# Performance work log

Hardware: AMD Instinct MI355X
Metric: run time of the kernel (lower is better)

The kernel has to match this reference:

```python
import jax, jax.numpy as jnp
import numpy as np

B, S, H, E, K = 4, 2048, 1024, 8, 2

def setup_inputs() -> dict:
    key = jax.random.key(0)
    k0, k1, k2, k3 = jax.random.split(key, 4)
    x = jax.random.normal(k0, (B, S, H), dtype=jnp.float32)
    # xavier-uniform-like scales
    router_w = jax.random.normal(k1, (E, H), dtype=jnp.float32) * np.float32(1.0 / np.sqrt(H))
    xav1 = np.float32(np.sqrt(2.0 / (2 * H + H)))
    w1 = jax.random.normal(k2, (E, 2 * H, H), dtype=jnp.float32) * xav1
    w2 = jax.random.normal(k3, (E, H, 2 * H), dtype=jnp.float32) * xav1
    return {"x": x, "router_w": router_w, "w1": w1, "w2": w2}

def reference(x, router_w, w1, w2):
    bsz, seq, hidden = x.shape
    n_experts = w1.shape[0]
    tokens = x.reshape(-1, hidden)                      # [T, H]
    T = tokens.shape[0]
    logits = tokens @ router_w.T                        # [T, E]
    topv, topi = jax.lax.top_k(logits, K)               # [T, K]
    w = jax.nn.softmax(topv, axis=-1).astype(tokens.dtype)
    # Dense gate matrix: gate[t, e] = routing weight of expert e for token t
    # (zero for non-selected experts). Equivalent to the torch pad/dispatch/
    # scatter-add combine: padded slots have weight 0 and contribute nothing.
    gate = jnp.zeros((T, n_experts), tokens.dtype).at[jnp.arange(T)[:, None], topi].add(w)
    out = jnp.zeros_like(tokens)
    for e in range(n_experts):  # small fixed expert count
        h = jax.nn.gelu(tokens @ w1[e].T, approximate=False)  # [T, 2H] (torch F.gelu = erf)
        y = h @ w2[e].T                                       # [T, H]
        out = out + gate[:, e:e + 1] * y
    return out.reshape(bsz, seq, hidden)
```

## Files before the change

### kernel.cpp

```cpp
#include <hip/hip_runtime.h>
#include <stdint.h>
#include <math.h>

#define T_TOK 8192
#define H_DIM 1024
#define H2    2048
#define NE    8

typedef unsigned short u16;
typedef __attribute__((ext_vector_type(8))) short bf16x8;
typedef __attribute__((ext_vector_type(4))) float f32x4;

__device__ __forceinline__ u16 f32_to_bf16(float f) {
  union { float f; unsigned u; } c; c.f = f;
  unsigned u = c.u + 0x7fffu + ((c.u >> 16) & 1u);
  return (u16)(u >> 16);
}
__device__ __forceinline__ float bf2f(u16 v) {
  union { unsigned u; float f; } c; c.u = (unsigned)v << 16; return c.f;
}

__device__ __forceinline__ float fast_gelu(float v) {
  float u = v * v;
  float z2 = v * fmaf(u, 0.1029437f, 2.3022078f);
  float e = __builtin_amdgcn_exp2f(z2);
  float r = __builtin_amdgcn_rcpf(1.0f + e);
  return v - v * r;
}

__device__ __forceinline__ void g2l16(const void* g, void* l) {
  __builtin_amdgcn_global_load_lds(
      (const __attribute__((address_space(1))) unsigned*)g,
      (__attribute__((address_space(3))) unsigned*)l, 16, 0, 0);
}

__device__ __forceinline__ int prefix_base(const int* counts, int e) {
  int b = 0;
#pragma unroll
  for (int j = 0; j < NE; j++) b += (j < e) ? counts[j] : 0;
  return b;
}

__global__ __launch_bounds__(256) void prep_kernel(
    const float* __restrict__ x, const float* __restrict__ rw,
    const float* __restrict__ w1, const float* __restrict__ w2,
    u16* __restrict__ xb, u16* __restrict__ w1b, u16* __restrict__ w2b,
    int* __restrict__ tope, float2* __restrict__ gate2,
    int* __restrict__ counts) {
  int blk = blockIdx.x;
  if (blk < T_TOK / 4) {
    int wave = threadIdx.x >> 6;
    int lane = threadIdx.x & 63;
    int t = blk * 4 + wave;
    const float4* x4 = (const float4*)(x + (size_t)t * H_DIM);
    const float4* rw4 = (const float4*)rw;
    u16* xbrow = xb + (size_t)t * H_DIM;

    double acc[NE];
#pragma unroll
    for (int e = 0; e < NE; e++) acc[e] = 0.0;
#pragma unroll
    for (int i = 0; i < 4; i++) {
      int c = lane + 64 * i;
      float4 xv = x4[c];
      ushort4 bv = make_ushort4(f32_to_bf16(xv.x), f32_to_bf16(xv.y),
                                f32_to_bf16(xv.z), f32_to_bf16(xv.w));
      *(ushort4*)(xbrow + c * 4) = bv;
#pragma unroll
      for (int e = 0; e < NE; e++) {
        float4 wv = rw4[e * 256 + c];
        acc[e] += (double)xv.x * wv.x + (double)xv.y * wv.y +
                  (double)xv.z * wv.z + (double)xv.w * wv.w;
      }
    }
#pragma unroll
    for (int off = 32; off >= 1; off >>= 1)
#pragma unroll
      for (int e = 0; e < NE; e++) acc[e] += __shfl_xor(acc[e], off, 64);

    if (lane == 0) {
      int e0 = 0; double v0 = acc[0];
#pragma unroll
      for (int e = 1; e < NE; e++) if (acc[e] > v0) { v0 = acc[e]; e0 = e; }
      int e1 = -1; double v1 = -1e300;
#pragma unroll
      for (int e = 0; e < NE; e++) if (e != e0 && acc[e] > v1) { v1 = acc[e]; e1 = e; }
      double ex = exp(v1 - v0);
      tope[t] = e0 | (e1 << 8);
      gate2[t] = make_float2((float)(1.0 / (1.0 + ex)), (float)(ex / (1.0 + ex)));
    }
  } else {
    int cb = blk - T_TOK / 4;
    if (cb == 0 && threadIdx.x < NE) counts[threadIdx.x] = 0;
    const float* src; u16* dst;
    if (cb < 3072) { src = w1; dst = w1b; }
    else           { src = w2; dst = w2b; cb -= 3072; }
    const int n4 = NE * H2 * H_DIM / 4;
    const int stride = 3072 * 256;
    const float4* s4 = (const float4*)src;
    for (int i = cb * 256 + threadIdx.x; i < n4; i += stride) {
      float4 v = s4[i];
      *(ushort4*)(dst + (size_t)i * 4) = make_ushort4(
          f32_to_bf16(v.x), f32_to_bf16(v.y), f32_to_bf16(v.z), f32_to_bf16(v.w));
    }
  }
}

__global__ __launch_bounds__(256) void build_kernel(
    const int* __restrict__ tope, int* __restrict__ counts,
    int* __restrict__ tok_list, int2* __restrict__ pos2) {
  __shared__ int cts[4][NE];
  __shared__ int gbase[NE];
  int tid = threadIdx.x, lane = tid & 63, w = tid >> 6;
  int t = blockIdx.x * 256 + tid;
  int pk = tope[t];
  int e0 = pk & 0xff, e1 = (pk >> 8) & 0xff;
  unsigned long long lt = ((unsigned long long)1 << lane) - 1;

  int r0 = 0, r1 = 0;
#pragma unroll
  for (int e = 0; e < NE; e++) {
    unsigned long long b0 = __ballot(e0 == e);
    unsigned long long b1 = __ballot(e1 == e);
    int n0 = __popcll(b0), n1 = __popcll(b1);
    if (e0 == e) r0 = __popcll(b0 & lt);
    if (e1 == e) r1 = n0 + __popcll(b1 & lt);
    if (lane == 0) cts[w][e] = n0 + n1;
  }
  __syncthreads();
  if (tid < NE) {
    int bt = cts[0][tid] + cts[1][tid] + cts[2][tid] + cts[3][tid];
    gbase[tid] = atomicAdd(&counts[tid], bt);
  }
  __syncthreads();
  int off0 = gbase[e0] + r0;
  int off1 = gbase[e1] + r1;
#pragma unroll
  for (int wp = 0; wp < 4; wp++) {
    if (wp < w) { off0 += cts[wp][e0]; off1 += cts[wp][e1]; }
  }
  tok_list[e0 * T_TOK + off0] = t;
  tok_list[e1 * T_TOK + off1] = t;
  pos2[t] = make_int2(off0, off1);
}

template <int NK, int NT, int OUTN, bool GATHER, bool GELU>
__global__ __launch_bounds__(512, 2) void moe_gemm(
    const u16* __restrict__ A, const u16* __restrict__ W,
    u16* __restrict__ O, const int* __restrict__ tok_list,
    const int* __restrict__ counts) {
  const int MTMAX = T_TOK / 256;
  int e = blockIdx.x / (MTMAX * NT);
  int rem = blockIdx.x % (MTMAX * NT);
  int mt = rem / NT, nt = rem % NT;
  int cnt = counts[e];
  int m0 = mt * 256;
  if (m0 >= cnt) return;
  int base = prefix_base(counts, e);
  const int K = NK * 32;

  __shared__ u16 lA[4][8192];
  __shared__ u16 lB[4][8192];

  int tid = threadIdx.x;
  int lane = tid & 63, wave = tid >> 6;
  int wr = wave >> 2, wc = wave & 3;
  int quad = lane >> 4, l16 = lane & 15;

  int cg = (tid & 3) ^ ((tid >> 3) & 3);
  const u16* We = W + (size_t)e * OUTN * K;
  const u16* asrc[2]; const u16* bsrc[2];
#pragma unroll
  for (int r = 0; r < 2; ++r) {
    int row = (tid >> 2) + 128 * r;
    int ar = m0 + row; if (ar > cnt - 1) ar = cnt - 1;
    if (GATHER) asrc[r] = A + (size_t)tok_list[e * T_TOK + ar] * K + cg * 8;
    else        asrc[r] = A + (size_t)(base + ar) * K + cg * 8;
    bsrc[r] = We + (size_t)(nt * 256 + row) * K + cg * 8;
  }

  auto stage = [&](int kt) {
    int b = kt & 3;
#pragma unroll
    for (int r = 0; r < 2; ++r) {
      g2l16(asrc[r] + kt * 32, &lA[b][r * 4096 + tid * 8]);
      g2l16(bsrc[r] + kt * 32, &lB[b][r * 4096 + tid * 8]);
    }
  };

  f32x4 acc[8][4];
#pragma unroll
  for (int i = 0; i < 8; i++)
#pragma unroll
    for (int j = 0; j < 4; j++)
#pragma unroll
      for (int r = 0; r < 4; r++) acc[i][j][r] = 0.f;

  stage(0); stage(1); stage(2);
  asm volatile("s_waitcnt vmcnt(8)" ::: "memory");
  __builtin_amdgcn_s_barrier();
  __builtin_amdgcn_sched_barrier(0);

  int aoff = (wr * 128 + l16) * 32 + (quad ^ ((l16 >> 1) & 3)) * 8;
  int boff = (wc * 64 + l16) * 32 + (quad ^ ((l16 >> 1) & 3)) * 8;

#pragma unroll 1
  for (int k = 0; k < NK; ++k) {
    const u16* Ab = &lA[k & 3][0] + aoff;
    const u16* Bb = &lB[k & 3][0] + boff;
    bf16x8 af[8], bfr[4];
#pragma unroll
    for (int mi = 0; mi < 8; ++mi)
      af[mi] = *(const bf16x8*)(Ab + mi * 512);
#pragma unroll
    for (int ni = 0; ni < 4; ++ni)
      bfr[ni] = *(const bf16x8*)(Bb + ni * 512);

    if (k + 3 < NK) stage(k + 3);

    __builtin_amdgcn_s_setprio(1);
#pragma unroll
    for (int mi = 0; mi < 8; ++mi)
#pragma unroll
      for (int ni = 0; ni < 4; ++ni)
        acc[mi][ni] = __builtin_amdgcn_mfma_f32_16x16x32_bf16(
            af[mi], bfr[ni], acc[mi][ni], 0, 0, 0);
    __builtin_amdgcn_s_setprio(0);

    if (k + 3 < NK)      asm volatile("s_waitcnt vmcnt(8)" ::: "memory");
    else if (k + 2 < NK) asm volatile("s_waitcnt vmcnt(4)" ::: "memory");
    else if (k + 1 < NK) asm volatile("s_waitcnt vmcnt(0)" ::: "memory");
    if (k + 1 < NK) {
      __builtin_amdgcn_s_barrier();
      __builtin_amdgcn_sched_barrier(0);
    }
  }

#pragma unroll
  for (int mi = 0; mi < 8; ++mi) {
    int rb = wr * 128 + mi * 16 + quad * 4;
#pragma unroll
    for (int r = 0; r < 4; ++r) {
      int grow = m0 + rb + r;
      if (grow < cnt) {
        size_t o = (size_t)(base + grow) * OUTN + nt * 256 + wc * 64 + l16;
#pragma unroll
        for (int ni = 0; ni < 4; ++ni) {
          float v = acc[mi][ni][r];
          if (GELU) v = fast_gelu(v);
          O[o + ni * 16] = f32_to_bf16(v);
        }
      }
    }
  }
}

__global__ __launch_bounds__(256) void combine_kernel(
    const u16* __restrict__ y, const int* __restrict__ tope,
    const float2* __restrict__ gate2, const int2* __restrict__ pos2,
    const int* __restrict__ counts, float* __restrict__ out) {
  int t = blockIdx.x;
  int pk = tope[t];
  int e0 = pk & 0xff, e1 = (pk >> 8) & 0xff;
  float2 g = gate2[t];
  int2 p = pos2[t];
  int hb0 = prefix_base(counts, e0);
  int hb1 = prefix_base(counts, e1);
  size_t s0 = (size_t)(hb0 + p.x) * H_DIM + threadIdx.x * 4;
  size_t s1 = (size_t)(hb1 + p.y) * H_DIM + threadIdx.x * 4;
  ushort4 a = *(const ushort4*)(y + s0);
  ushort4 b = *(const ushort4*)(y + s1);
  float4 o;
  o.x = g.x * bf2f(a.x) + g.y * bf2f(b.x);
  o.y = g.x * bf2f(a.y) + g.y * bf2f(b.y);
  o.z = g.x * bf2f(a.z) + g.y * bf2f(b.z);
  o.w = g.x * bf2f(a.w) + g.y * bf2f(b.w);
  *(float4*)(out + (size_t)t * H_DIM + threadIdx.x * 4) = o;
}

extern "C" void kernel_launch(void* const* d_in, const int* in_sizes, int n_in,
                              void* d_out, int out_size, void* d_ws, size_t ws_size,
                              hipStream_t stream) {
  const float* x  = (const float*)d_in[0];
  const float* rw = (const float*)d_in[1];
  const float* w1 = (const float*)d_in[2];
  const float* w2 = (const float*)d_in[3];
  float* out = (float*)d_out;

  char* ws = (char*)d_ws;
  u16* xb       = (u16*)(ws);
  u16* w1b      = (u16*)(ws + 16777216);
  u16* y        = (u16*)(ws + 16777216);
  u16* w2b      = (u16*)(ws + 50331648);
  u16* h        = (u16*)(ws + 83886080);
  int* tok_list = (int*)(ws + 150994944);
  int* tope     = (int*)(ws + 151257088);
  float2* gate2 = (float2*)(ws + 151289856);
  int2* pos2    = (int2*)(ws + 151355392);
  int* counts   = (int*)(ws + 151420928);

  prep_kernel<<<T_TOK / 4 + 6144, 256, 0, stream>>>(x, rw, w1, w2, xb, w1b, w2b,
                                                    tope, gate2, counts);
  build_kernel<<<T_TOK / 256, 256, 0, stream>>>(tope, counts, tok_list, pos2);
  moe_gemm<32, 8, H2, true, true>
      <<<NE * 32 * 8, 512, 0, stream>>>(xb, w1b, h, tok_list, counts);
  moe_gemm<64, 4, H_DIM, false, false>
      <<<NE * 32 * 4, 512, 0, stream>>>(h, w2b, y, tok_list, counts);
  combine_kernel<<<T_TOK, 256, 0, stream>>>(y, tope, gate2, pos2, counts, out);
}
```

Measured before the change: 400.8 us.

## Restructure expert GEMM main loop into half-tile double-buffered ping-pong schedule

The expert GEMM now uses 64-wide K tiles and two LDS buffers, each split into halves, replacing the previous 4-stage ring of 32-wide K tiles. Each K tile is processed as four quarter MFMA blocks. Global-to-LDS loads for later halves are issued between these blocks, with barriers fencing each block, so memory traffic overlaps compute at a finer grain. LDS addressing uses a new XOR swizzle over 8 chunks per row. The change adds many more barriers per tile and relies on precise vmcnt accounting, which could cost more in synchronisation than the overlap gains.

```diff
diff --git a/kernel.cpp b/kernel.cpp
--- a/kernel.cpp
+++ b/kernel.cpp
@@ -144,7 +144,66 @@
   pos2[t] = make_int2(off0, off1);
 }
 
-template <int NK, int NT, int OUTN, bool GATHER, bool GELU>
+#define SB  __builtin_amdgcn_sched_barrier(0)
+#define BAR() do { SB; __builtin_amdgcn_s_barrier(); SB; } while (0)
+#define VMW(N) asm volatile("s_waitcnt vmcnt(" #N ")" ::: "memory")
+
+#define LDA(D,H,F,KK) (*(const bf16x8*)&lA[(((D)*2+(H))<<13) + adA[F][KK]])
+#define LDB(D,H,J,KK) (*(const bf16x8*)&lB[(((D)*2+(H))<<13) + adB[J][KK]])
+
+#define RDA(D,H) do { _Pragma("unroll") \
+  for (int f_ = 0; f_ < 4; ++f_) { af[f_][0] = LDA(D,H,f_,0); af[f_][1] = LDA(D,H,f_,1); } } while (0)
+#define RDB(D,H,BP) do { \
+  BP[0][0]=LDB(D,H,0,0); BP[0][1]=LDB(D,H,0,1); \
+  BP[1][0]=LDB(D,H,1,0); BP[1][1]=LDB(D,H,1,1); } while (0)
+
+#define STGA(D,H,KT) do { \
+  g2l16(aptr[H][0] + (KT)*64, &lA[(((D)*2+(H))<<13) + sd0]); \
+  g2l16(aptr[H][1] + (KT)*64, &lA[(((D)*2+(H))<<13) + sd1]); } while (0)
+#define STGB(D,H,KT) do { \
+  g2l16(bptr[H][0] + (KT)*64, &lB[(((D)*2+(H))<<13) + sd0]); \
+  g2l16(bptr[H][1] + (KT)*64, &lB[(((D)*2+(H))<<13) + sd1]); } while (0)
+
+#define MMQ(FB, BP, NB) do { \
+  __builtin_amdgcn_s_setprio(1); \
+  _Pragma("unroll") \
+  for (int f_ = 0; f_ < 4; ++f_) \
+    _Pragma("unroll") \
+    for (int j_ = 0; j_ < 2; ++j_) \
+      _Pragma("unroll") \
+      for (int k_ = 0; k_ < 2; ++k_) \
+        acc[(FB)+f_][(NB)+j_] = __builtin_amdgcn_mfma_f32_16x16x32_bf16( \
+            af[f_][k_], BP[j_][k_], acc[(FB)+f_][(NB)+j_], 0, 0, 0); \
+  __builtin_amdgcn_s_setprio(0); \
+} while (0)
+
+#define TILE_FULL(D, KT) do { \
+  RDA(D,0); RDB(D,0,b0); SB; STGA(((D)^1), 1, (KT)+1); \
+  BAR(); MMQ(0, b0, 0); BAR(); \
+  RDB(D,1,b1); SB; STGA(D, 0, (KT)+2); \
+  BAR(); MMQ(0, b1, 2); BAR(); \
+  RDA(D,1); SB; STGB(D, 0, (KT)+2); \
+  BAR(); MMQ(4, b0, 0); BAR(); \
+  SB; STGB(D, 1, (KT)+2); \
+  BAR(); MMQ(4, b1, 2); VMW(6); BAR(); \
+} while (0)
+
+#define TILE_TAIL1(D, KT) do { \
+  RDA(D,0); RDB(D,0,b0); SB; STGA(((D)^1), 1, (KT)+1); \
+  BAR(); MMQ(0, b0, 0); BAR(); \
+  RDB(D,1,b1); BAR(); MMQ(0, b1, 2); BAR(); \
+  RDA(D,1); BAR(); MMQ(4, b0, 0); BAR(); \
+  MMQ(4, b1, 2); VMW(0); BAR(); \
+} while (0)
+
+#define TILE_TAIL0(D) do { \
+  RDA(D,0); RDB(D,0,b0); BAR(); MMQ(0, b0, 0); BAR(); \
+  RDB(D,1,b1); BAR(); MMQ(0, b1, 2); BAR(); \
+  RDA(D,1); BAR(); MMQ(4, b0, 0); BAR(); \
+  MMQ(4, b1, 2); \
+} while (0)
+
+template <int NKT, int NT, int OUTN, bool GATHER, bool GELU>
 __global__ __launch_bounds__(512, 2) void moe_gemm(
     const u16* __restrict__ A, const u16* __restrict__ W,
     u16* __restrict__ O, const int* __restrict__ tok_list,
@@ -157,36 +216,53 @@
   int m0 = mt * 256;
   if (m0 >= cnt) return;
   int base = prefix_base(counts, e);
-  const int K = NK * 32;
-
-  __shared__ u16 lA[4][8192];
-  __shared__ u16 lB[4][8192];
+  const int K = NKT * 64;
+
+  __shared__ u16 lA[32768];
+  __shared__ u16 lB[32768];
 
   int tid = threadIdx.x;
-  int lane = tid & 63, wave = tid >> 6;
-  int wr = wave >> 2, wc = wave & 3;
-  int quad = lane >> 4, l16 = lane & 15;
-
-  int cg = (tid & 3) ^ ((tid >> 3) & 3);
+  int ln = tid & 63, w = tid >> 6;
+  int wr = w >> 2, wc = w & 3;
+  int quad = ln >> 4, l16 = ln & 15;
+
+  int sd0 = w * 1024 + ln * 8;
+  int sd1 = sd0 + 512;
   const u16* We = W + (size_t)e * OUTN * K;
-  const u16* asrc[2]; const u16* bsrc[2];
-#pragma unroll
-  for (int r = 0; r < 2; ++r) {
-    int row = (tid >> 2) + 128 * r;
-    int ar = m0 + row; if (ar > cnt - 1) ar = cnt - 1;
-    if (GATHER) asrc[r] = A + (size_t)tok_list[e * T_TOK + ar] * K + cg * 8;
-    else        asrc[r] = A + (size_t)(base + ar) * K + cg * 8;
-    bsrc[r] = We + (size_t)(nt * 256 + row) * K + cg * 8;
-  }
-
-  auto stage = [&](int kt) {
-    int b = kt & 3;
-#pragma unroll
-    for (int r = 0; r < 2; ++r) {
-      g2l16(asrc[r] + kt * 32, &lA[b][r * 4096 + tid * 8]);
-      g2l16(bsrc[r] + kt * 32, &lB[b][r * 4096 + tid * 8]);
-    }
-  };
+  const u16* aptr[2][2]; const u16* bptr[2][2];
+#pragma unroll
+  for (int c = 0; c < 2; ++c) {
+    int j16 = w * 128 + c * 64 + ln;
+    int lr = j16 >> 3;
+    int chunk = (j16 & 7) ^ (lr & 7);
+#pragma unroll
+    for (int h = 0; h < 2; ++h) {
+      int arow = ((lr >> 6) << 7) + h * 64 + (lr & 63);
+      int ar = m0 + arow; if (ar > cnt - 1) ar = cnt - 1;
+      const u16* ab;
+      if (GATHER) ab = A + (size_t)tok_list[e * T_TOK + ar] * K;
+      else        ab = A + (size_t)(base + ar) * K;
+      aptr[h][c] = ab + chunk * 8;
+      int brow = ((lr >> 5) << 6) + h * 32 + (lr & 31);
+      bptr[h][c] = We + (size_t)(nt * 256 + brow) * K + chunk * 8;
+    }
+  }
+
+  int adA[4][2], adB[2][2];
+#pragma unroll
+  for (int f = 0; f < 4; ++f) {
+    int lr = wr * 64 + f * 16 + l16;
+#pragma unroll
+    for (int kk = 0; kk < 2; ++kk)
+      adA[f][kk] = lr * 64 + ((((kk << 2) | quad) ^ (lr & 7)) << 3);
+  }
+#pragma unroll
+  for (int j = 0; j < 2; ++j) {
+    int lr = wc * 32 + j * 16 + l16;
+#pragma unroll
+    for (int kk = 0; kk < 2; ++kk)
+      adB[j][kk] = lr * 64 + ((((kk << 2) | quad) ^ (lr & 7)) << 3);
+  }
 
   f32x4 acc[8][4];
 #pragma unroll
@@ -196,45 +272,20 @@
 #pragma unroll
       for (int r = 0; r < 4; r++) acc[i][j][r] = 0.f;
 
-  stage(0); stage(1); stage(2);
-  asm volatile("s_waitcnt vmcnt(8)" ::: "memory");
-  __builtin_amdgcn_s_barrier();
-  __builtin_amdgcn_sched_barrier(0);
-
-  int aoff = (wr * 128 + l16) * 32 + (quad ^ ((l16 >> 1) & 3)) * 8;
-  int boff = (wc * 64 + l16) * 32 + (quad ^ ((l16 >> 1) & 3)) * 8;
+  bf16x8 af[4][2], b0[2][2], b1[2][2];
+
+  STGA(0,0,0); STGB(0,0,0); STGB(0,1,0); STGA(0,1,0);
+  STGA(1,0,1); STGB(1,0,1); STGB(1,1,1);
+  VMW(6);
+  BAR();
 
 #pragma unroll 1
-  for (int k = 0; k < NK; ++k) {
-    const u16* Ab = &lA[k & 3][0] + aoff;
-    const u16* Bb = &lB[k & 3][0] + boff;
-    bf16x8 af[8], bfr[4];
-#pragma unroll
-    for (int mi = 0; mi < 8; ++mi)
-      af[mi] = *(const bf16x8*)(Ab + mi * 512);
-#pragma unroll
-    for (int ni = 0; ni < 4; ++ni)
-      bfr[ni] = *(const bf16x8*)(Bb + ni * 512);
-
-    if (k + 3 < NK) stage(k + 3);
-
-    __builtin_amdgcn_s_setprio(1);
-#pragma unroll
-    for (int mi = 0; mi < 8; ++mi)
-#pragma unroll
-      for (int ni = 0; ni < 4; ++ni)
-        acc[mi][ni] = __builtin_amdgcn_mfma_f32_16x16x32_bf16(
-            af[mi], bfr[ni], acc[mi][ni], 0, 0, 0);
-    __builtin_amdgcn_s_setprio(0);
-
-    if (k + 3 < NK)      asm volatile("s_waitcnt vmcnt(8)" ::: "memory");
-    else if (k + 2 < NK) asm volatile("s_waitcnt vmcnt(4)" ::: "memory");
-    else if (k + 1 < NK) asm volatile("s_waitcnt vmcnt(0)" ::: "memory");
-    if (k + 1 < NK) {
-      __builtin_amdgcn_s_barrier();
-      __builtin_amdgcn_sched_barrier(0);
-    }
-  }
+  for (int t = 0; t < NKT - 2; t += 2) {
+    TILE_FULL(0, t);
+    TILE_FULL(1, t + 1);
+  }
+  TILE_TAIL1(0, NKT - 2);
+  TILE_TAIL0(1);
 
 #pragma unroll
   for (int mi = 0; mi < 8; ++mi) {
@@ -302,9 +353,9 @@
   prep_kernel<<<T_TOK / 4 + 6144, 256, 0, stream>>>(x, rw, w1, w2, xb, w1b, w2b,
                                                     tope, gate2, counts);
   build_kernel<<<T_TOK / 256, 256, 0, stream>>>(tope, counts, tok_list, pos2);
-  moe_gemm<32, 8, H2, true, true>
+  moe_gemm<16, 8, H2, true, true>
       <<<NE * 32 * 8, 512, 0, stream>>>(xb, w1b, h, tok_list, counts);
-  moe_gemm<64, 4, H_DIM, false, false>
+  moe_gemm<32, 4, H_DIM, false, false>
       <<<NE * 32 * 4, 512, 0, stream>>>(h, w2b, y, tok_list, counts);
   combine_kernel<<<T_TOK, 256, 0, stream>>>(y, tope, gate2, pos2, counts, out);
 }
```

New measurement: 403.1 us. No clear change (+0.6%).

## Switch MoE GEMM to 64-wide K tiles with double buffering and expert-interleaved blocks

Applied to the files above, without the earlier changes.

The grouped GEMM now stages 64-element K tiles with a 2-stage double buffer instead of 32-element tiles in a 4-stage ring. The LDS layout uses an 8-chunk XOR swizzle with precomputed fragment addresses. Block indexing is changed so the expert is the fastest-varying index, which spreads active blocks across experts. Each iteration issues twice the MFMAs per barrier, halving barrier count, but the wait is now a full vmcnt(0), so latency hiding depends on one tile of prefetch only.

```diff
diff --git a/kernel.cpp b/kernel.cpp
--- a/kernel.cpp
+++ b/kernel.cpp
@@ -144,49 +144,58 @@
   pos2[t] = make_int2(off0, off1);
 }
 
-template <int NK, int NT, int OUTN, bool GATHER, bool GELU>
+template <int NKT, int NT, int OUTN, bool GATHER, bool GELU>
 __global__ __launch_bounds__(512, 2) void moe_gemm(
     const u16* __restrict__ A, const u16* __restrict__ W,
     u16* __restrict__ O, const int* __restrict__ tok_list,
     const int* __restrict__ counts) {
-  const int MTMAX = T_TOK / 256;
-  int e = blockIdx.x / (MTMAX * NT);
-  int rem = blockIdx.x % (MTMAX * NT);
+  int e = blockIdx.x & 7;
+  int rem = blockIdx.x >> 3;
   int mt = rem / NT, nt = rem % NT;
   int cnt = counts[e];
   int m0 = mt * 256;
   if (m0 >= cnt) return;
   int base = prefix_base(counts, e);
-  const int K = NK * 32;
-
-  __shared__ u16 lA[4][8192];
-  __shared__ u16 lB[4][8192];
+  const int K = NKT * 64;
+
+  __shared__ u16 lA[2][16384];
+  __shared__ u16 lB[2][16384];
 
   int tid = threadIdx.x;
-  int lane = tid & 63, wave = tid >> 6;
-  int wr = wave >> 2, wc = wave & 3;
-  int quad = lane >> 4, l16 = lane & 15;
-
-  int cg = (tid & 3) ^ ((tid >> 3) & 3);
+  int ln = tid & 63, w = tid >> 6;
+  int wr = w >> 2, wc = w & 3;
+  int quad = ln >> 4, l16 = ln & 15;
+
   const u16* We = W + (size_t)e * OUTN * K;
-  const u16* asrc[2]; const u16* bsrc[2];
-#pragma unroll
-  for (int r = 0; r < 2; ++r) {
-    int row = (tid >> 2) + 128 * r;
+  const u16* aptr[4]; const u16* bptr[4];
+#pragma unroll
+  for (int c = 0; c < 4; ++c) {
+    int u = c * 512 + tid;
+    int row = u >> 3;
+    int chunk = (u & 7) ^ (row & 7);
     int ar = m0 + row; if (ar > cnt - 1) ar = cnt - 1;
-    if (GATHER) asrc[r] = A + (size_t)tok_list[e * T_TOK + ar] * K + cg * 8;
-    else        asrc[r] = A + (size_t)(base + ar) * K + cg * 8;
-    bsrc[r] = We + (size_t)(nt * 256 + row) * K + cg * 8;
-  }
-
-  auto stage = [&](int kt) {
-    int b = kt & 3;
-#pragma unroll
-    for (int r = 0; r < 2; ++r) {
-      g2l16(asrc[r] + kt * 32, &lA[b][r * 4096 + tid * 8]);
-      g2l16(bsrc[r] + kt * 32, &lB[b][r * 4096 + tid * 8]);
-    }
-  };
+    const u16* ab;
+    if (GATHER) ab = A + (size_t)tok_list[e * T_TOK + ar] * K;
+    else        ab = A + (size_t)(base + ar) * K;
+    aptr[c] = ab + chunk * 8;
+    bptr[c] = We + (size_t)(nt * 256 + row) * K + chunk * 8;
+  }
+
+  int adA[8][2], adB[4][2];
+#pragma unroll
+  for (int f = 0; f < 8; ++f) {
+    int r = wr * 128 + f * 16 + l16;
+#pragma unroll
+    for (int kk = 0; kk < 2; ++kk)
+      adA[f][kk] = r * 64 + ((((kk << 2) | quad) ^ (r & 7)) << 3);
+  }
+#pragma unroll
+  for (int j = 0; j < 4; ++j) {
+    int r = wc * 64 + j * 16 + l16;
+#pragma unroll
+    for (int kk = 0; kk < 2; ++kk)
+      adB[j][kk] = r * 64 + ((((kk << 2) | quad) ^ (r & 7)) << 3);
+  }
 
   f32x4 acc[8][4];
 #pragma unroll
@@ -196,44 +205,57 @@
 #pragma unroll
       for (int r = 0; r < 4; r++) acc[i][j][r] = 0.f;
 
-  stage(0); stage(1); stage(2);
-  asm volatile("s_waitcnt vmcnt(8)" ::: "memory");
-  __builtin_amdgcn_s_barrier();
-  __builtin_amdgcn_sched_barrier(0);
-
-  int aoff = (wr * 128 + l16) * 32 + (quad ^ ((l16 >> 1) & 3)) * 8;
-  int boff = (wc * 64 + l16) * 32 + (quad ^ ((l16 >> 1) & 3)) * 8;
+#pragma unroll
+  for (int c = 0; c < 4; ++c) {
+    g2l16(aptr[c], &lA[0][(c * 512 + tid) * 8]);
+    g2l16(bptr[c], &lB[0][(c * 512 + tid) * 8]);
+  }
 
 #pragma unroll 1
-  for (int k = 0; k < NK; ++k) {
-    const u16* Ab = &lA[k & 3][0] + aoff;
-    const u16* Bb = &lB[k & 3][0] + boff;
-    bf16x8 af[8], bfr[4];
-#pragma unroll
-    for (int mi = 0; mi < 8; ++mi)
-      af[mi] = *(const bf16x8*)(Ab + mi * 512);
-#pragma unroll
-    for (int ni = 0; ni < 4; ++ni)
-      bfr[ni] = *(const bf16x8*)(Bb + ni * 512);
-
-    if (k + 3 < NK) stage(k + 3);
+  for (int t = 0; t < NKT; ++t) {
+    int d = t & 1;
+    asm volatile("s_waitcnt vmcnt(0)" ::: "memory");
+    __builtin_amdgcn_s_barrier();
+    __builtin_amdgcn_sched_barrier(0);
+
+    const u16* Ab = &lA[d][0];
+    const u16* Bb = &lB[d][0];
+    bf16x8 af[8], af2[8], bf[4], bf2v[4];
+    af[0]  = *(const bf16x8*)(Ab + adA[0][0]);
+    af2[0] = *(const bf16x8*)(Ab + adA[0][1]);
+#pragma unroll
+    for (int j = 0; j < 4; ++j) {
+      bf[j]   = *(const bf16x8*)(Bb + adB[j][0]);
+      bf2v[j] = *(const bf16x8*)(Bb + adB[j][1]);
+    }
+#pragma unroll
+    for (int f = 1; f < 8; ++f) {
+      af[f]  = *(const bf16x8*)(Ab + adA[f][0]);
+      af2[f] = *(const bf16x8*)(Ab + adA[f][1]);
+    }
+
+    if (t + 1 < NKT) {
+#pragma unroll
+      for (int c = 0; c < 4; ++c) {
+        g2l16(aptr[c] + (t + 1) * 64, &lA[d ^ 1][(c * 512 + tid) * 8]);
+        g2l16(bptr[c] + (t + 1) * 64, &lB[d ^ 1][(c * 512 + tid) * 8]);
+      }
+    }
+    __builtin_amdgcn_sched_barrier(0);
 
     __builtin_amdgcn_s_setprio(1);
 #pragma unroll
-    for (int mi = 0; mi < 8; ++mi)
+    for (int mi = 0; mi < 8; ++mi) {
 #pragma unroll
       for (int ni = 0; ni < 4; ++ni)
         acc[mi][ni] = __builtin_amdgcn_mfma_f32_16x16x32_bf16(
-            af[mi], bfr[ni], acc[mi][ni], 0, 0, 0);
+            af[mi], bf[ni], acc[mi][ni], 0, 0, 0);
+#pragma unroll
+      for (int ni = 0; ni < 4; ++ni)
+        acc[mi][ni] = __builtin_amdgcn_mfma_f32_16x16x32_bf16(
+            af2[mi], bf2v[ni], acc[mi][ni], 0, 0, 0);
+    }
     __builtin_amdgcn_s_setprio(0);
-
-    if (k + 3 < NK)      asm volatile("s_waitcnt vmcnt(8)" ::: "memory");
-    else if (k + 2 < NK) asm volatile("s_waitcnt vmcnt(4)" ::: "memory");
-    else if (k + 1 < NK) asm volatile("s_waitcnt vmcnt(0)" ::: "memory");
-    if (k + 1 < NK) {
-      __builtin_amdgcn_s_barrier();
-      __builtin_amdgcn_sched_barrier(0);
-    }
   }
 
 #pragma unroll
@@ -302,9 +324,9 @@
   prep_kernel<<<T_TOK / 4 + 6144, 256, 0, stream>>>(x, rw, w1, w2, xb, w1b, w2b,
                                                     tope, gate2, counts);
   build_kernel<<<T_TOK / 256, 256, 0, stream>>>(tope, counts, tok_list, pos2);
-  moe_gemm<32, 8, H2, true, true>
+  moe_gemm<16, 8, H2, true, true>
       <<<NE * 32 * 8, 512, 0, stream>>>(xb, w1b, h, tok_list, counts);
-  moe_gemm<64, 4, H_DIM, false, false>
+  moe_gemm<32, 4, H_DIM, false, false>
       <<<NE * 32 * 4, 512, 0, stream>>>(h, w2b, y, tok_list, counts);
   combine_kernel<<<T_TOK, 256, 0, stream>>>(y, tope, gate2, pos2, counts, out);
 }
```

Result: faster. 390.7 us (-2.5%).
